# Performance work log

Measured on AMD Instinct MI355X. Metric: run time of the kernel, lower is better.

## Reference

```python
import jax, jax.numpy as jnp
import numpy as np

HIDDEN = 2048
KEY_DIM = 2048
NUM_HEADS = 16
HEAD_DIM = KEY_DIM // NUM_HEADS
ROPE_THETA = 10000.0
EPS = 1e-05


def rms_norm(x, w, eps=EPS):
    var = jnp.mean(x * x, axis=-1, keepdims=True)
    return x * jax.lax.rsqrt(var + eps) * w


def apply_rope(x, theta_base=ROPE_THETA):
    # x: [b, s, h, d]; faithful to the einops repeat '(2 d)' = tile (concat), with
    # even output positions = cos*x1 - sin*x2, odd = sin*x1 + cos*x2.
    b, s, h, d = x.shape
    half = d // 2
    freqs = theta_base ** (jnp.arange(half, dtype=x.dtype) * (-2.0 / d))  # [d/2]
    freqs = jnp.concatenate([freqs, freqs], axis=-1)                      # [d] (tiled)
    pos = jnp.arange(s, dtype=x.dtype)                                    # [s]
    ang = pos[:, None] * freqs[None, :]                                   # [s, d]
    cos = jnp.cos(ang)[None, :, None, :]
    sin = jnp.sin(ang)[None, :, None, :]
    x_even = x[..., 0::2]
    x_odd = x[..., 1::2]
    x1 = jnp.concatenate([x_even, x_even], axis=-1)  # tile '(2 d)'
    x2 = jnp.concatenate([x_odd, x_odd], axis=-1)
    even_mask = (jnp.arange(d) % 2 == 0)[None, None, None, :]
    return jnp.where(even_mask, cos * x1 - sin * x2, sin * x1 + cos * x2)


def setup_inputs() -> dict:
    key = jax.random.key(0)
    ks = jax.random.split(key, 10)
    B, S = 2, 2048
    s_in = 1.0 / np.sqrt(HIDDEN)
    s_k = 1.0 / np.sqrt(KEY_DIM)
    return {
        "x": jax.random.normal(ks[0], (B, S, HIDDEN), dtype=jnp.float32),
        "rms_w": jnp.ones((HIDDEN,), dtype=jnp.float32),
        "wq": jax.random.normal(ks[1], (HIDDEN, KEY_DIM), dtype=jnp.float32) * s_in,
        "bq": jnp.zeros((KEY_DIM,), dtype=jnp.float32),
        "wk": jax.random.normal(ks[2], (HIDDEN, KEY_DIM), dtype=jnp.float32) * s_in,
        "bk": jnp.zeros((KEY_DIM,), dtype=jnp.float32),
        "wv": jax.random.normal(ks[3], (HIDDEN, KEY_DIM), dtype=jnp.float32) * s_in,
        "bv": jnp.zeros((KEY_DIM,), dtype=jnp.float32),
        "wo": jax.random.normal(ks[4], (KEY_DIM, HIDDEN), dtype=jnp.float32) * s_k,
        "bo": jnp.zeros((HIDDEN,), dtype=jnp.float32),
    }


def reference(x, rms_w, wq, bq, wk, bk, wv, bv, wo, bo):
    B, S, _ = x.shape
    residual = x
    xn = rms_norm(x, rms_w)
    q = (xn @ wq + bq).reshape(B, S, NUM_HEADS, HEAD_DIM)
    k = (xn @ wk + bk).reshape(B, S, NUM_HEADS, HEAD_DIM)
    v = (xn @ wv + bv).reshape(B, S, NUM_HEADS, HEAD_DIM)
    q = apply_rope(q)
    k = apply_rope(k)
    scores = jnp.einsum('bshd,bthd->bhst', q, k) / jnp.sqrt(
        jnp.asarray(HEAD_DIM, dtype=x.dtype))
    causal = jnp.tril(jnp.ones((S, S), dtype=bool))[None, None]
    scores = jnp.where(causal, scores, -jnp.inf)
    probs = jax.nn.softmax(scores, axis=-1)
    out = jnp.einsum('bhst,bthd->bshd', probs, v).reshape(B, S, KEY_DIM)
    return out @ wo + bo + residual
```

## Files before the change

### kernel.cpp

```cpp
#include <hip/hip_runtime.h>
#include <stdint.h>
#include <math.h>

#define S_LEN 2048
#define HID 2048
#define NH 16
#define HD 128
#define NROWS 4096
#define SCALE 0.08838834764831845f
#define C2 (0.08838834764831845f * 1.442695040888963f)

typedef unsigned short u16;
typedef __attribute__((ext_vector_type(8))) short short8;
typedef __attribute__((ext_vector_type(4))) float f32x4;
typedef __attribute__((ext_vector_type(16))) float f32x16;
typedef __attribute__((ext_vector_type(4))) unsigned short u16x4;
typedef __attribute__((ext_vector_type(4))) unsigned int u32x4;
typedef __attribute__((ext_vector_type(4))) float float4v;

__device__ __forceinline__ u16 f2bf(float f) {
  union { float f; uint32_t u; } v; v.f = f;
  uint32_t r = v.u + 0x7FFFu + ((v.u >> 16) & 1u);
  return (u16)(r >> 16);
}
__device__ __forceinline__ float bf2f(u16 b) {
  union { uint32_t u; float f; } v; v.u = ((uint32_t)b) << 16;
  return v.f;
}
__device__ __forceinline__ void gl_lds16(const void* g, void* l) {
  __builtin_amdgcn_global_load_lds((const __attribute__((address_space(1))) void*)g,
                                   (__attribute__((address_space(3))) void*)l, 16, 0, 0);
}
__device__ __forceinline__ unsigned cvtpk(float lo, float hi) {
  unsigned r;
  asm("v_cvt_pk_bf16_f32 %0, %1, %2" : "=v"(r) : "v"(lo), "v"(hi));
  return r;
}
__device__ __forceinline__ void plswap(unsigned &a, unsigned &b) {
  asm volatile("v_permlane32_swap_b32 %0, %1" : "+v"(a), "+v"(b));
}

__global__ __launch_bounds__(256) void k_rmsnorm(const float* __restrict__ x,
                                                 const float* __restrict__ w,
                                                 u16* __restrict__ xn) {
  int row = blockIdx.x;
  int tid = threadIdx.x;
  const float* xr = x + (size_t)row * HID;
  float4v a = *(const float4v*)(xr + tid * 8);
  float4v b = *(const float4v*)(xr + tid * 8 + 4);
  float s = a[0]*a[0] + a[1]*a[1] + a[2]*a[2] + a[3]*a[3]
          + b[0]*b[0] + b[1]*b[1] + b[2]*b[2] + b[3]*b[3];
  #pragma unroll
  for (int off = 1; off < 64; off <<= 1) s += __shfl_xor(s, off, 64);
  __shared__ float red[4];
  int wv = tid >> 6;
  if ((tid & 63) == 0) red[wv] = s;
  __syncthreads();
  float tot = red[0] + red[1] + red[2] + red[3];
  float r = rsqrtf(tot * (1.0f / HID) + 1e-5f);
  const float* wp = w + tid * 8;
  u16x4 o0, o1;
  #pragma unroll
  for (int j = 0; j < 4; ++j) { o0[j] = f2bf(a[j] * r * wp[j]); o1[j] = f2bf(b[j] * r * wp[4 + j]); }
  *(u16x4*)(xn + (size_t)row * HID + tid * 8) = o0;
  *(u16x4*)(xn + (size_t)row * HID + tid * 8 + 4) = o1;
}

__global__ __launch_bounds__(256) void k_wconv4(const float* __restrict__ w0, const float* __restrict__ w1,
                                                const float* __restrict__ w2, const float* __restrict__ w3,
                                                u16* __restrict__ wtbase) {
  int z = blockIdx.z;
  const float* w = (z == 0) ? w0 : (z == 1) ? w1 : (z == 2) ? w2 : w3;
  u16* wt = wtbase + (size_t)z * HID * HID;
  int n0 = blockIdx.x * 64, k0 = blockIdx.y * 64;
  __shared__ float t[64][68];
  int tid = threadIdx.x;
  int cr = tid >> 4;
  int cc = (tid & 15) * 4;
  #pragma unroll
  for (int it = 0; it < 4; ++it) {
    int kk = cr + it * 16;
    float4v v = *(const float4v*)(w + (size_t)(k0 + kk) * HID + n0 + cc);
    t[kk][cc] = v[0]; t[kk][cc + 1] = v[1]; t[kk][cc + 2] = v[2]; t[kk][cc + 3] = v[3];
  }
  __syncthreads();
  #pragma unroll
  for (int it = 0; it < 4; ++it) {
    int nn = cr + it * 16;
    u16x4 o;
    #pragma unroll
    for (int j = 0; j < 4; ++j) o[j] = f2bf(t[cc + j][nn]);
    *(u16x4*)(wt + (size_t)(n0 + nn) * HID + k0 + cc) = o;
  }
}

__global__ __launch_bounds__(256) void k_ropepack(const u16* __restrict__ qh, const u16* __restrict__ kh,
                                                  u16* __restrict__ QP, u16* __restrict__ KP) {
  int tid = threadIdx.x;
  int l = tid & 63, wvv = tid >> 6;
  int rsub = l >> 4, c = l & 15;
  int row = blockIdx.x * 16 + wvv * 4 + rsub;
  int bh = row >> 11, s = row & 2047;
  int tile = s >> 5, ln = s & 31;
  int ks = c >> 1, hi = c & 1;
  int k3 = ks & 3;
  const u16* qi = qh + (size_t)row * HD + 32 * k3 + 16 * hi;
  const u16* ki = kh + (size_t)row * HD + 32 * k3 + 16 * hi;
  float sn[8], cs[8];
  #pragma unroll
  for (int j = 0; j < 8; ++j) {
    int de = 16 * k3 + 8 * hi + j;
    float freq = exp2f((float)de * -0.20762050593046014f);
    sincosf((float)s * freq, &sn[j], &cs[j]);
  }
  size_t off = ((((size_t)(bh * 64 + tile)) * 8 + ks) * 64 + hi * 32 + ln) * 8;
  {
    short8 a = *(const short8*)(qi);
    short8 b2 = *(const short8*)(qi + 8);
    u16x4 o0, o1;
    #pragma unroll
    for (int j = 0; j < 4; ++j) {
      float x0 = bf2f((u16)a[2 * j]), x1 = bf2f((u16)a[2 * j + 1]);
      o0[j] = f2bf((j & 1) ? (sn[j] * x0 + cs[j] * x1) : (cs[j] * x0 - sn[j] * x1));
    }
    #pragma unroll
    for (int j = 0; j < 4; ++j) {
      int jj = j + 4;
      float x0 = bf2f((u16)b2[2 * j]), x1 = bf2f((u16)b2[2 * j + 1]);
      o1[j] = f2bf((jj & 1) ? (sn[jj] * x0 + cs[jj] * x1) : (cs[jj] * x0 - sn[jj] * x1));
    }
    *(u16x4*)(QP + off) = o0; *(u16x4*)(QP + off + 4) = o1;
  }
  {
    short8 a = *(const short8*)(ki);
    short8 b2 = *(const short8*)(ki + 8);
    u16x4 o0, o1;
    #pragma unroll
    for (int j = 0; j < 4; ++j) {
      float x0 = bf2f((u16)a[2 * j]), x1 = bf2f((u16)a[2 * j + 1]);
      o0[j] = f2bf((j & 1) ? (sn[j] * x0 + cs[j] * x1) : (cs[j] * x0 - sn[j] * x1));
    }
    #pragma unroll
    for (int j = 0; j < 4; ++j) {
      int jj = j + 4;
      float x0 = bf2f((u16)b2[2 * j]), x1 = bf2f((u16)b2[2 * j + 1]);
      o1[j] = f2bf((jj & 1) ? (sn[jj] * x0 + cs[jj] * x1) : (cs[jj] * x0 - sn[jj] * x1));
    }
    *(u16x4*)(KP + off) = o0; *(u16x4*)(KP + off + 4) = o1;
  }
}

__global__ __launch_bounds__(256) void k_vpack(const u16* __restrict__ vh, u16* __restrict__ VP) {
  int bx = blockIdx.x;
  int bh = blockIdx.y;
  __shared__ u16 t[64][136];
  int tid = threadIdx.x;
  int row = tid >> 2;
  int d0 = (tid & 3) * 32;
  const u16* src = vh + ((size_t)bh * S_LEN + bx * 64 + row) * HD + d0;
  short8 a = *(const short8*)(src);
  short8 b = *(const short8*)(src + 8);
  short8 c = *(const short8*)(src + 16);
  short8 d = *(const short8*)(src + 24);
  *(short8*)(&t[row][d0]) = a;
  *(short8*)(&t[row][d0 + 8]) = b;
  *(short8*)(&t[row][d0 + 16]) = c;
  *(short8*)(&t[row][d0 + 24]) = d;
  __syncthreads();
  #pragma unroll
  for (int i = 0; i < 4; ++i) {
    int cc = i * 256 + tid;
    int lp = cc & 63;
    int db = (cc >> 6) & 3;
    int j2 = (cc >> 8) & 1;
    int tl = (cc >> 9) & 1;
    int tg = bx * 2 + tl;
    int tloc = tl * 32 + j2 * 16 + (lp >> 5) * 8;
    int dloc = db * 32 + (lp & 31);
    short8 v;
    #pragma unroll
    for (int jj = 0; jj < 8; ++jj) v[jj] = (short)t[tloc + jj][dloc];
    size_t off = ((((size_t)(bh * 64 + tg) * 2 + j2) * 4 + db) * 64 + lp) * 8;
    *(short8*)(VP + off) = v;
  }
}

__global__ __launch_bounds__(512, 2) void k_gemm_qkv2(const u16* __restrict__ A, const u16* __restrict__ BT,
                                                      const float* __restrict__ bq, const float* __restrict__ bk,
                                                      const float* __restrict__ bv, u16* __restrict__ qkv) {
  extern __shared__ __align__(16) char smraw[];
  u16* sm = (u16*)smraw;
  int bid = blockIdx.x;
  int xcd = bid & 7, loc = bid >> 3;
  int bx = xcd * 3 + loc % 3;
  int by = loc / 3;
  int tid = threadIdx.x;
  int w = tid >> 6, lane = tid & 63;
  int wr = w >> 2, wc = w & 3;
  int lq = lane & 15, lg = lane >> 4;

  f32x4 acc[4][4];
  #pragma unroll
  for (int mi = 0; mi < 4; ++mi)
    #pragma unroll
    for (int ni = 0; ni < 4; ++ni) acc[mi][ni] = (f32x4){0.f, 0.f, 0.f, 0.f};

  const size_t Abase = (size_t)(by * 128) * HID;
  const size_t Bbase = (size_t)(bx * 256) * HID;

  #define STAGE_Q(n)  do { \
    int slot_ = ((n) & 3) * 12288; \
    int kb_ = (n) * 32; \
    { int c_ = tid; int row_ = c_ >> 2; int ch_ = (c_ & 3) ^ (row_ & 3); \
      gl_lds16(A + Abase + (size_t)row_ * HID + kb_ + ch_ * 8, sm + slot_ + c_ * 8); } \
    _Pragma("unroll") \
    for (int it_ = 0; it_ < 2; ++it_) { \
      int c_ = it_ * 512 + tid; int row_ = c_ >> 2; int ch_ = (c_ & 3) ^ (row_ & 3); \
      gl_lds16(BT + Bbase + (size_t)row_ * HID + kb_ + ch_ * 8, sm + slot_ + 4096 + c_ * 8); } \
  } while (0)

  STAGE_Q(0); STAGE_Q(1); STAGE_Q(2); STAGE_Q(3);
  asm volatile("s_waitcnt vmcnt(6)" ::: "memory");
  __builtin_amdgcn_s_barrier();
  __builtin_amdgcn_sched_barrier(0);

  for (int n = 0; n < 64; ++n) {
    if (n >= 1 && n <= 60) STAGE_Q(n + 3);
    int slot = (n & 3) * 12288;
    const u16* sA = sm + slot;
    const u16* sB = sm + slot + 4096;
    short8 af[4], bf[4];
    #pragma unroll
    for (int mi = 0; mi < 4; ++mi) {
      int ra = wr * 64 + mi * 16 + lq;
      af[mi] = *(const short8*)(sA + ra * 32 + ((lg ^ (ra & 3)) << 3));
    }
    #pragma unroll
    for (int ni = 0; ni < 4; ++ni) {
      int rb = wc * 64 + ni * 16 + lq;
      bf[ni] = *(const short8*)(sB + rb * 32 + ((lg ^ (rb & 3)) << 3));
    }
    __builtin_amdgcn_s_setprio(1);
    #pragma unroll
    for (int mi = 0; mi < 4; ++mi)
      #pragma unroll
      for (int ni = 0; ni < 4; ++ni)
        acc[mi][ni] = __builtin_amdgcn_mfma_f32_16x16x32_bf16(af[mi], bf[ni], acc[mi][ni], 0, 0, 0);
    __builtin_amdgcn_s_setprio(0);
    if (n <= 60)      asm volatile("s_waitcnt vmcnt(6)" ::: "memory");
    else if (n == 61) asm volatile("s_waitcnt vmcnt(3)" ::: "memory");
    else              asm volatile("s_waitcnt vmcnt(0)" ::: "memory");
    __builtin_amdgcn_s_barrier();
    __builtin_amdgcn_sched_barrier(0);
  }

  #pragma unroll
  for (int ni = 0; ni < 4; ++ni) {
    int colg = bx * 256 + wc * 64 + ni * 16 + lq;
    int sel = colg >> 11;
    int col = colg & 2047;
    int h = col >> 7, d = col & 127;
    const float* bias = (sel == 0) ? bq : (sel == 1) ? bk : bv;
    float bs = bias[col];
    u16* outp = qkv + (size_t)sel * NROWS * HID;
    #pragma unroll
    for (int mi = 0; mi < 4; ++mi) {
      #pragma unroll
      for (int r = 0; r < 4; ++r) {
        int rowm = by * 128 + wr * 64 + mi * 16 + lg * 4 + r;
        int b = rowm >> 11, s = rowm & 2047;
        outp[(((size_t)(b * NH + h)) * S_LEN + s) * HD + d] = f2bf(acc[mi][ni][r] + bs);
      }
    }
  }
  #undef STAGE_Q
}

__global__ __launch_bounds__(512, 2) void k_gemm_o2(const u16* __restrict__ A, const u16* __restrict__ BT,
                                                    const float* __restrict__ bias,
                                                    const float* __restrict__ resid,
                                                    float* __restrict__ outp) {
  extern __shared__ __align__(16) char smraw[];
  u16* sm = (u16*)smraw;
  int bid = blockIdx.x;
  int bx = bid & 7;
  int by = bid >> 3;
  int tid = threadIdx.x;
  int w = tid >> 6, lane = tid & 63;
  int wr = w >> 2, wc = w & 3;
  int lq = lane & 15, lg = lane >> 4;

  f32x4 acc[4][4];
  #pragma unroll
  for (int mi = 0; mi < 4; ++mi)
    #pragma unroll
    for (int ni = 0; ni < 4; ++ni) acc[mi][ni] = (f32x4){0.f, 0.f, 0.f, 0.f};

  const size_t Abase = (size_t)(by * 128) * HID;
  const size_t Bbase = (size_t)(bx * 256) * HID;

  #define STAGE_O(n)  do { \
    int slot_ = ((n) & 3) * 12288; \
    int kb_ = (n) * 32; \
    { int c_ = tid; int row_ = c_ >> 2; int ch_ = (c_ & 3) ^ (row_ & 3); \
      gl_lds16(A + Abase + (size_t)row_ * HID + kb_ + ch_ * 8, sm + slot_ + c_ * 8); } \
    _Pragma("unroll") \
    for (int it_ = 0; it_ < 2; ++it_) { \
      int c_ = it_ * 512 + tid; int row_ = c_ >> 2; int ch_ = (c_ & 3) ^ (row_ & 3); \
      gl_lds16(BT + Bbase + (size_t)row_ * HID + kb_ + ch_ * 8, sm + slot_ + 4096 + c_ * 8); } \
  } while (0)

  STAGE_O(0); STAGE_O(1); STAGE_O(2); STAGE_O(3);
  asm volatile("s_waitcnt vmcnt(6)" ::: "memory");
  __builtin_amdgcn_s_barrier();
  __builtin_amdgcn_sched_barrier(0);

  for (int n = 0; n < 64; ++n) {
    if (n >= 1 && n <= 60) STAGE_O(n + 3);
    int slot = (n & 3) * 12288;
    const u16* sA = sm + slot;
    const u16* sB = sm + slot + 4096;
    short8 af[4], bf[4];
    #pragma unroll
    for (int mi = 0; mi < 4; ++mi) {
      int ra = wr * 64 + mi * 16 + lq;
      af[mi] = *(const short8*)(sA + ra * 32 + ((lg ^ (ra & 3)) << 3));
    }
    #pragma unroll
    for (int ni = 0; ni < 4; ++ni) {
      int rb = wc * 64 + ni * 16 + lq;
      bf[ni] = *(const short8*)(sB + rb * 32 + ((lg ^ (rb & 3)) << 3));
    }
    __builtin_amdgcn_s_setprio(1);
    #pragma unroll
    for (int mi = 0; mi < 4; ++mi)
      #pragma unroll
      for (int ni = 0; ni < 4; ++ni)
        acc[mi][ni] = __builtin_amdgcn_mfma_f32_16x16x32_bf16(af[mi], bf[ni], acc[mi][ni], 0, 0, 0);
    __builtin_amdgcn_s_setprio(0);
    if (n <= 60)      asm volatile("s_waitcnt vmcnt(6)" ::: "memory");
    else if (n == 61) asm volatile("s_waitcnt vmcnt(3)" ::: "memory");
    else              asm volatile("s_waitcnt vmcnt(0)" ::: "memory");
    __builtin_amdgcn_s_barrier();
    __builtin_amdgcn_sched_barrier(0);
  }

  #pragma unroll
  for (int ni = 0; ni < 4; ++ni) {
    int col = bx * 256 + wc * 64 + ni * 16 + lq;
    float bs = bias[col];
    #pragma unroll
    for (int mi = 0; mi < 4; ++mi) {
      #pragma unroll
      for (int r = 0; r < 4; ++r) {
        int rowm = by * 128 + wr * 64 + mi * 16 + lg * 4 + r;
        size_t o = (size_t)rowm * HID + col;
        outp[o] = acc[mi][ni][r] + bs + resid[o];
      }
    }
  }
  #undef STAGE_O
}

__global__ __launch_bounds__(64, 2) void k_attn(const u16* __restrict__ QP, const u16* __restrict__ KP,
                                                const u16* __restrict__ VP, u16* __restrict__ out) {
  int bid = blockIdx.x;
  int rest = bid >> 3;
  int bh = (bid & 7) * 4 + (rest & 3);
  int gg = rest >> 2;
  int qw = (gg < 32) ? (63 - gg) : (gg - 32);
  int b = bh >> 4, h = bh & 15;
  int lane = threadIdx.x;
  int hi = lane >> 5, ln = lane & 31;
  int q0 = qw * 32, qrow = q0 + ln;

  const u16* QPb = QP + ((size_t)(bh * 64 + qw) * 8) * 512 + lane * 8;
  short8 qf[8];
  #pragma unroll
  for (int ks = 0; ks < 8; ++ks) qf[ks] = *(const short8*)(QPb + ks * 512);

  f32x16 oc[4];
  #pragma unroll
  for (int db = 0; db < 4; ++db)
    #pragma unroll
    for (int r = 0; r < 16; ++r) oc[db][r] = 0.f;
  float mr = -3.0e38f, l = 0.f;

  const u16* KPb = KP + ((size_t)bh * 64 * 8) * 512 + lane * 8;
  const u16* VPb = VP + ((size_t)bh * 64 * 8) * 512 + lane * 8;

  int ntile = qw + 1;
  short8 kf[8];
  #pragma unroll
  for (int ks = 0; ks < 8; ++ks) kf[ks] = *(const short8*)(KPb + ks * 512);

  for (int tt = 0; tt < ntile; ++tt) {
    short8 va[8];
    #pragma unroll
    for (int u = 0; u < 8; ++u) va[u] = *(const short8*)(VPb + (size_t)tt * 4096 + u * 512);

    f32x16 st;
    #pragma unroll
    for (int r = 0; r < 16; ++r) st[r] = 0.f;
    __builtin_amdgcn_s_setprio(1);
    #pragma unroll
    for (int ks = 0; ks < 8; ++ks)
      st = __builtin_amdgcn_mfma_f32_32x32x16_bf16(kf[ks], qf[ks], st, 0, 0, 0);
    __builtin_amdgcn_s_setprio(0);

    if (tt + 1 < ntile) {
      #pragma unroll
      for (int ks = 0; ks < 8; ++ks)
        kf[ks] = *(const short8*)(KPb + (size_t)(tt + 1) * 4096 + ks * 512);
    }

    int t0 = tt * 32;
    float sv[16];
    float pm = -3.0e38f;
    bool lastt = (tt == ntile - 1);
    #pragma unroll
    for (int r = 0; r < 16; ++r) {
      float x = st[r];
      if (lastt) {
        int t = t0 + (r & 3) + 8 * (r >> 2) + 4 * hi;
        x = (t <= qrow) ? x : -3.0e38f;
      }
      sv[r] = x;
    }
    #pragma unroll
    for (int r = 0; r < 15; r += 2) pm = fmaxf(fmaxf(pm, sv[r]), sv[r + 1]);
    pm = fmaxf(pm, sv[15]);
    pm = fmaxf(pm, __shfl_xor(pm, 32, 64));
    if (!__all(pm <= mr + 64.0f)) {
      float mnew = fmaxf(mr, pm);
      float al = exp2f((mr - mnew) * C2);
      l *= al;
      #pragma unroll
      for (int db = 0; db < 4; ++db)
        #pragma unroll
        for (int r = 0; r < 16; ++r) oc[db][r] *= al;
      mr = mnew;
    }
    float mc = mr * C2;
    float e[16];
    float rs = 0.f;
    #pragma unroll
    for (int r = 0; r < 16; ++r) {
      e[r] = exp2f(fmaf(sv[r], C2, -mc));
      rs += e[r];
    }
    rs += __shfl_xor(rs, 32, 64);
    l += rs;

    unsigned w0 = cvtpk(e[0], e[1]),   w1 = cvtpk(e[2], e[3]);
    unsigned w2 = cvtpk(e[4], e[5]),   w3 = cvtpk(e[6], e[7]);
    unsigned w4 = cvtpk(e[8], e[9]),   w5 = cvtpk(e[10], e[11]);
    unsigned w6 = cvtpk(e[12], e[13]), w7 = cvtpk(e[14], e[15]);
    plswap(w0, w2); plswap(w1, w3); plswap(w4, w6); plswap(w5, w7);
    u32x4 pw0 = {w0, w1, w2, w3};
    u32x4 pw1 = {w4, w5, w6, w7};
    short8 pb0 = __builtin_bit_cast(short8, pw0);
    short8 pb1 = __builtin_bit_cast(short8, pw1);

    __builtin_amdgcn_s_setprio(1);
    #pragma unroll
    for (int db = 0; db < 4; ++db)
      oc[db] = __builtin_amdgcn_mfma_f32_32x32x16_bf16(va[db], pb0, oc[db], 0, 0, 0);
    #pragma unroll
    for (int db = 0; db < 4; ++db)
      oc[db] = __builtin_amdgcn_mfma_f32_32x32x16_bf16(va[4 + db], pb1, oc[db], 0, 0, 0);
    __builtin_amdgcn_s_setprio(0);
  }

  float inv = 1.0f / l;
  size_t ob = ((size_t)(b * S_LEN + qrow)) * HID + h * HD;
  #pragma unroll
  for (int db = 0; db < 4; ++db) {
    #pragma unroll
    for (int g = 0; g < 4; ++g) {
      u16x4 pk;
      #pragma unroll
      for (int j = 0; j < 4; ++j) pk[j] = f2bf(oc[db][4 * g + j] * inv);
      *(u16x4*)(out + ob + db * 32 + 8 * g + 4 * hi) = pk;
    }
  }
}

extern "C" void kernel_launch(void* const* d_in, const int* in_sizes, int n_in,
                              void* d_out, int out_size, void* d_ws, size_t ws_size,
                              hipStream_t stream) {
  const float* x    = (const float*)d_in[0];
  const float* rmsw = (const float*)d_in[1];
  const float* wq   = (const float*)d_in[2];
  const float* bq   = (const float*)d_in[3];
  const float* wk   = (const float*)d_in[4];
  const float* bk   = (const float*)d_in[5];
  const float* wv   = (const float*)d_in[6];
  const float* bv   = (const float*)d_in[7];
  const float* wo   = (const float*)d_in[8];
  const float* bo   = (const float*)d_in[9];

  char* ws = (char*)d_ws;
  const size_t SZ = (size_t)NROWS * HID * 2;
  const size_t WSZ = (size_t)HID * HID * 2;
  u16* xn   = (u16*)(ws);
  u16* wqkT = (u16*)(ws + SZ);
  u16* woT  = (u16*)(ws + SZ + 3 * WSZ);
  u16* qhm  = (u16*)(ws + SZ + 4 * WSZ);
  u16* khm  = (u16*)(ws + SZ + 4 * WSZ + SZ);
  u16* vhm  = (u16*)(ws + SZ + 4 * WSZ + 2 * SZ);
  u16* QP   = xn;
  u16* KP   = wqkT;
  u16* VP   = khm;
  u16* ao   = qhm;

  k_rmsnorm<<<dim3(NROWS), dim3(256), 0, stream>>>(x, rmsw, xn);
  k_wconv4<<<dim3(32, 32, 4), dim3(256), 0, stream>>>(wq, wk, wv, wo, wqkT);
  k_gemm_qkv2<<<dim3(768), dim3(512), 98304, stream>>>(xn, wqkT, bq, bk, bv, qhm);
  k_ropepack<<<dim3(4096), dim3(256), 0, stream>>>(qhm, khm, QP, KP);
  k_vpack<<<dim3(32, 32), dim3(256), 0, stream>>>(vhm, VP);
  k_attn<<<dim3(2048), dim3(64), 0, stream>>>(QP, KP, VP, ao);
  k_gemm_o2<<<dim3(256), dim3(512), 98304, stream>>>(ao, woT, bo, x, (float*)d_out);
}
```

Baseline: 280.9 us.

## Switch GEMM LDS pipeline to triple buffering with row-pair XOR swizzle

Both bf16 MFMA GEMMs move from a 4-slot, 3-ahead LDS prefetch ring to a 3-slot, 2-ahead ring. Dynamic shared memory drops from 96KB to 72KB, so more blocks can share a CU (two per CU within 160KB LDS). The XOR swizzle now keys on (row>>1)&3 instead of row&3, meant to cut LDS bank conflicts on the 16-byte fragment reads. In exchange, the prefetch distance is shorter, so global load latency is less well hidden, and the final iteration drops its barrier.

```diff
diff --git a/kernel.cpp b/kernel.cpp
--- a/kernel.cpp
+++ b/kernel.cpp
@@ -209,36 +209,36 @@
   const size_t Bbase = (size_t)(bx * 256) * HID;
 
   #define STAGE_Q(n)  do { \
-    int slot_ = ((n) & 3) * 12288; \
+    int slot_ = ((n) % 3) * 12288; \
     int kb_ = (n) * 32; \
-    { int c_ = tid; int row_ = c_ >> 2; int ch_ = (c_ & 3) ^ (row_ & 3); \
+    { int c_ = tid; int row_ = c_ >> 2; int ch_ = (c_ & 3) ^ ((row_ >> 1) & 3); \
       gl_lds16(A + Abase + (size_t)row_ * HID + kb_ + ch_ * 8, sm + slot_ + c_ * 8); } \
     _Pragma("unroll") \
     for (int it_ = 0; it_ < 2; ++it_) { \
-      int c_ = it_ * 512 + tid; int row_ = c_ >> 2; int ch_ = (c_ & 3) ^ (row_ & 3); \
+      int c_ = it_ * 512 + tid; int row_ = c_ >> 2; int ch_ = (c_ & 3) ^ ((row_ >> 1) & 3); \
       gl_lds16(BT + Bbase + (size_t)row_ * HID + kb_ + ch_ * 8, sm + slot_ + 4096 + c_ * 8); } \
   } while (0)
 
-  STAGE_Q(0); STAGE_Q(1); STAGE_Q(2); STAGE_Q(3);
-  asm volatile("s_waitcnt vmcnt(6)" ::: "memory");
+  STAGE_Q(0); STAGE_Q(1);
+  asm volatile("s_waitcnt vmcnt(3)" ::: "memory");
   __builtin_amdgcn_s_barrier();
   __builtin_amdgcn_sched_barrier(0);
 
   for (int n = 0; n < 64; ++n) {
-    if (n >= 1 && n <= 60) STAGE_Q(n + 3);
-    int slot = (n & 3) * 12288;
+    if (n + 2 <= 63) STAGE_Q(n + 2);
+    int slot = (n % 3) * 12288;
     const u16* sA = sm + slot;
     const u16* sB = sm + slot + 4096;
     short8 af[4], bf[4];
     #pragma unroll
     for (int mi = 0; mi < 4; ++mi) {
       int ra = wr * 64 + mi * 16 + lq;
-      af[mi] = *(const short8*)(sA + ra * 32 + ((lg ^ (ra & 3)) << 3));
+      af[mi] = *(const short8*)(sA + ra * 32 + ((lg ^ ((ra >> 1) & 3)) << 3));
     }
     #pragma unroll
     for (int ni = 0; ni < 4; ++ni) {
       int rb = wc * 64 + ni * 16 + lq;
-      bf[ni] = *(const short8*)(sB + rb * 32 + ((lg ^ (rb & 3)) << 3));
+      bf[ni] = *(const short8*)(sB + rb * 32 + ((lg ^ ((rb >> 1) & 3)) << 3));
     }
     __builtin_amdgcn_s_setprio(1);
     #pragma unroll
@@ -247,11 +247,15 @@
       for (int ni = 0; ni < 4; ++ni)
         acc[mi][ni] = __builtin_amdgcn_mfma_f32_16x16x32_bf16(af[mi], bf[ni], acc[mi][ni], 0, 0, 0);
     __builtin_amdgcn_s_setprio(0);
-    if (n <= 60)      asm volatile("s_waitcnt vmcnt(6)" ::: "memory");
-    else if (n == 61) asm volatile("s_waitcnt vmcnt(3)" ::: "memory");
-    else              asm volatile("s_waitcnt vmcnt(0)" ::: "memory");
-    __builtin_amdgcn_s_barrier();
-    __builtin_amdgcn_sched_barrier(0);
+    if (n <= 61) {
+      asm volatile("s_waitcnt vmcnt(3)" ::: "memory");
+      __builtin_amdgcn_s_barrier();
+      __builtin_amdgcn_sched_barrier(0);
+    } else if (n == 62) {
+      asm volatile("s_waitcnt vmcnt(0)" ::: "memory");
+      __builtin_amdgcn_s_barrier();
+      __builtin_amdgcn_sched_barrier(0);
+    }
   }
 
   #pragma unroll
@@ -300,36 +304,36 @@
   const size_t Bbase = (size_t)(bx * 256) * HID;
 
   #define STAGE_O(n)  do { \
-    int slot_ = ((n) & 3) * 12288; \
+    int slot_ = ((n) % 3) * 12288; \
     int kb_ = (n) * 32; \
-    { int c_ = tid; int row_ = c_ >> 2; int ch_ = (c_ & 3) ^ (row_ & 3); \
+    { int c_ = tid; int row_ = c_ >> 2; int ch_ = (c_ & 3) ^ ((row_ >> 1) & 3); \
       gl_lds16(A + Abase + (size_t)row_ * HID + kb_ + ch_ * 8, sm + slot_ + c_ * 8); } \
     _Pragma("unroll") \
     for (int it_ = 0; it_ < 2; ++it_) { \
-      int c_ = it_ * 512 + tid; int row_ = c_ >> 2; int ch_ = (c_ & 3) ^ (row_ & 3); \
+      int c_ = it_ * 512 + tid; int row_ = c_ >> 2; int ch_ = (c_ & 3) ^ ((row_ >> 1) & 3); \
       gl_lds16(BT + Bbase + (size_t)row_ * HID + kb_ + ch_ * 8, sm + slot_ + 4096 + c_ * 8); } \
   } while (0)
 
-  STAGE_O(0); STAGE_O(1); STAGE_O(2); STAGE_O(3);
-  asm volatile("s_waitcnt vmcnt(6)" ::: "memory");
+  STAGE_O(0); STAGE_O(1);
+  asm volatile("s_waitcnt vmcnt(3)" ::: "memory");
   __builtin_amdgcn_s_barrier();
   __builtin_amdgcn_sched_barrier(0);
 
   for (int n = 0; n < 64; ++n) {
-    if (n >= 1 && n <= 60) STAGE_O(n + 3);
-    int slot = (n & 3) * 12288;
+    if (n + 2 <= 63) STAGE_O(n + 2);
+    int slot = (n % 3) * 12288;
     const u16* sA = sm + slot;
     const u16* sB = sm + slot + 4096;
     short8 af[4], bf[4];
     #pragma unroll
     for (int mi = 0; mi < 4; ++mi) {
       int ra = wr * 64 + mi * 16 + lq;
-      af[mi] = *(const short8*)(sA + ra * 32 + ((lg ^ (ra & 3)) << 3));
+      af[mi] = *(const short8*)(sA + ra * 32 + ((lg ^ ((ra >> 1) & 3)) << 3));
     }
     #pragma unroll
     for (int ni = 0; ni < 4; ++ni) {
       int rb = wc * 64 + ni * 16 + lq;
-      bf[ni] = *(const short8*)(sB + rb * 32 + ((lg ^ (rb & 3)) << 3));
+      bf[ni] = *(const short8*)(sB + rb * 32 + ((lg ^ ((rb >> 1) & 3)) << 3));
     }
     __builtin_amdgcn_s_setprio(1);
     #pragma unroll
@@ -338,11 +342,15 @@
       for (int ni = 0; ni < 4; ++ni)
         acc[mi][ni] = __builtin_amdgcn_mfma_f32_16x16x32_bf16(af[mi], bf[ni], acc[mi][ni], 0, 0, 0);
     __builtin_amdgcn_s_setprio(0);
-    if (n <= 60)      asm volatile("s_waitcnt vmcnt(6)" ::: "memory");
-    else if (n == 61) asm volatile("s_waitcnt vmcnt(3)" ::: "memory");
-    else              asm volatile("s_waitcnt vmcnt(0)" ::: "memory");
-    __builtin_amdgcn_s_barrier();
-    __builtin_amdgcn_sched_barrier(0);
+    if (n <= 61) {
+      asm volatile("s_waitcnt vmcnt(3)" ::: "memory");
+      __builtin_amdgcn_s_barrier();
+      __builtin_amdgcn_sched_barrier(0);
+    } else if (n == 62) {
+      asm volatile("s_waitcnt vmcnt(0)" ::: "memory");
+      __builtin_amdgcn_s_barrier();
+      __builtin_amdgcn_sched_barrier(0);
+    }
   }
 
   #pragma unroll
@@ -516,9 +524,9 @@
 
   k_rmsnorm<<<dim3(NROWS), dim3(256), 0, stream>>>(x, rmsw, xn);
   k_wconv4<<<dim3(32, 32, 4), dim3(256), 0, stream>>>(wq, wk, wv, wo, wqkT);
-  k_gemm_qkv2<<<dim3(768), dim3(512), 98304, stream>>>(xn, wqkT, bq, bk, bv, qhm);
+  k_gemm_qkv2<<<dim3(768), dim3(512), 73728, stream>>>(xn, wqkT, bq, bk, bv, qhm);
   k_ropepack<<<dim3(4096), dim3(256), 0, stream>>>(qhm, khm, QP, KP);
   k_vpack<<<dim3(32, 32), dim3(256), 0, stream>>>(vhm, VP);
   k_attn<<<dim3(2048), dim3(64), 0, stream>>>(QP, KP, VP, ao);
-  k_gemm_o2<<<dim3(256), dim3(512), 98304, stream>>>(ao, woT, bo, x, (float*)d_out);
-}
+  k_gemm_o2<<<dim3(256), dim3(512), 73728, stream>>>(ao, woT, bo, x, (float*)d_out);
+}
```

Measured after the change: 267.2 us. 4.9% less time.
